# Kernel tuning notes

Measured on AMD Instinct MI355X. Metric: run time of the kernel, lower is better.

## Reference

```python
import jax, jax.numpy as jnp
import numpy as np

N, E, F, H = 50000, 1600000, 128, 128  # nodes, edges, input_nf, hidden_nf


def setup_inputs() -> dict:
    key = jax.random.key(0)
    ks = jax.random.split(key, 16)
    s = 0.05
    inp = {
        "h": jax.random.normal(ks[0], (N, F), jnp.float32),
        "coord": jax.random.normal(ks[1], (N, 3), jnp.float32),
        "edge_index": jax.random.randint(ks[2], (2, E), 0, N, jnp.int32),
        # edge_mlp: Linear(2F+1, H) -> SiLU -> Linear(H, H) -> SiLU
        "We1": jax.random.normal(ks[3], (2 * F + 1, H), jnp.float32) * s,
        "be1": jnp.zeros((H,), jnp.float32),
        "We2": jax.random.normal(ks[4], (H, H), jnp.float32) * s,
        "be2": jnp.zeros((H,), jnp.float32),
        # node_mlp: Linear(H+F, H) -> SiLU -> Linear(H, F)
        "Wn1": jax.random.normal(ks[5], (H + F, H), jnp.float32) * s,
        "bn1": jnp.zeros((H,), jnp.float32),
        "Wn2": jax.random.normal(ks[6], (H, F), jnp.float32) * s,
        "bn2": jnp.zeros((F,), jnp.float32),
        # coord_mlp: Linear(H, H) -> SiLU -> Linear(H, 1, bias=False) (xavier gain 0.001)
        "Wc1": jax.random.normal(ks[7], (H, H), jnp.float32) * s,
        "bc1": jnp.zeros((H,), jnp.float32),
        "Wc2": jax.random.normal(ks[8], (H, 1), jnp.float32) * 0.001,
    }
    return inp


def reference(h, coord, edge_index, We1, be1, We2, be2, Wn1, bn1, Wn2, bn2, Wc1, bc1, Wc2):
    row, col = edge_index[0], edge_index[1]
    n = h.shape[0]

    # coord2radial (normalize=False)
    coord_diff = coord[row] - coord[col]                      # [E, 3]
    radial = jnp.sum(coord_diff * coord_diff, axis=1, keepdims=True)  # [E, 1]

    # edge_model (attention=False, edge_attr=None)
    e_in = jnp.concatenate([h[row], h[col], radial], axis=1)  # [E, 2F+1]
    edge_feat = jax.nn.silu(jax.nn.silu(e_in @ We1 + be1) @ We2 + be2)  # [E, H]

    # coord_model (coords_agg='mean', reflection_equiv=True, tanh=False)
    phi = jax.nn.silu(edge_feat @ Wc1 + bc1) @ Wc2            # [E, 1]
    trans = coord_diff * phi                                   # [E, 3]
    agg_c = jax.ops.segment_sum(trans, row, num_segments=n)    # [N, 3]
    cnt = jax.ops.segment_sum(jnp.ones((trans.shape[0], 1), trans.dtype), row, num_segments=n)
    coord_out = coord + agg_c / jnp.maximum(cnt, 1.0)

    # node_model (node_attr=None, residual=True)
    agg_h = jax.ops.segment_sum(edge_feat, row, num_segments=n)  # [N, H]
    n_in = jnp.concatenate([h, agg_h], axis=1)                   # [N, F+H]
    h_out = h + (jax.nn.silu(n_in @ Wn1 + bn1) @ Wn2 + bn2)

    return h_out, coord_out
```

## Files before the change

### kernel.cpp

```cpp
#include <hip/hip_runtime.h>


typedef float f32x4 __attribute__((ext_vector_type(4)));
typedef short s16x8 __attribute__((ext_vector_type(8)));

#define NN   50000
#define EE   1600000
#define NHF  6400000
#define NBIN 50000
#define NT   25000

__device__ __forceinline__ unsigned short f2bf(float x){
  union { float f; unsigned int u; } v; v.f = x;
  unsigned int r = v.u + 0x7fffu + ((v.u >> 16) & 1u);
  return (unsigned short)(r >> 16);
}
__device__ __forceinline__ unsigned int pack2(float a, float b){
  unsigned int r;
  asm("v_cvt_pk_bf16_f32 %0, %1, %2" : "=v"(r) : "v"(a), "v"(b));
  return r;
}
__device__ __forceinline__ float silu_f(float x){
  return x * __builtin_amdgcn_rcpf(1.f + __expf(-x));
}
__device__ __forceinline__ float bflo(unsigned int u){ return __uint_as_float(u << 16); }
__device__ __forceinline__ float bfhi(unsigned int u){ return __uint_as_float(u & 0xffff0000u); }

__device__ __forceinline__ f32x4 mfma16(s16x8 a, s16x8 b, f32x4 c){
  return __builtin_amdgcn_mfma_f32_16x16x32_bf16(a, b, c, 0, 0, 0);
}

template<int CTRL> __device__ __forceinline__ float dppf(float x){
  return __int_as_float(__builtin_amdgcn_update_dpp(0, __float_as_int(x), CTRL, 0xF, 0xF, true));
}
template<int CTRL> __device__ __forceinline__ int dppi(int x){
  return __builtin_amdgcn_update_dpp(-1, x, CTRL, 0xF, 0xF, false);
}

__device__ __forceinline__ short* sptr(short* base, int fi, int slot){
  return (short*)((char*)base + (fi << 10) + (((slot << 4) ^ ((fi & 3) << 5))));
}

__global__ void pack_weights(const float* __restrict__ We1, const float* __restrict__ We2,
                             const float* __restrict__ Wc1, const float* __restrict__ Wn1,
                             const float* __restrict__ Wn2, short* __restrict__ wp)
{
  int b = blockIdx.x;
  int m = b >> 5, t = b & 31;
  int ft = t >> 2, ks = t & 3;
  int lane = threadIdx.x;
  const float* src;
  switch (m) {
    case 0: src = We1;            break;
    case 1: src = We1 + 128*128;  break;
    case 2: src = We2;            break;
    case 3: src = Wc1;            break;
    case 4: src = Wn1;            break;
    case 5: src = Wn1 + 128*128;  break;
    default: src = Wn2;           break;
  }
  short* dst = wp + m*16384 + (((ft<<2) + ks)*64 + lane)*8;
  int f  = (ft<<4) + (lane & 15);
  int kb = (ks<<5) + ((lane >> 4) << 3);
#pragma unroll
  for (int j = 0; j < 8; ++j)
    dst[j] = (short)f2bf(src[(kb + j)*128 + f]);
}

__global__ __launch_bounds__(256, 2)
void a1_kernel(const float* __restrict__ h32, const short* __restrict__ wp,
               unsigned short* __restrict__ A1)
{
  __shared__ short sA[16][64][8];
  const int tid = threadIdx.x, w = tid >> 6, lane = tid & 63;
  const int n0 = blockIdx.x << 6;
  const int el = tid >> 2, q = tid & 3;
  const int fi0 = ((el >> 4) << 2) + q, er = el & 15;
  {
    const int node = n0 + el;
    if (node < NN) {
      const float* hp = h32 + (size_t)node*128 + q*32;
#pragma unroll
      for (int lg = 0; lg < 4; ++lg) {
        f32x4 u = *(const f32x4*)(hp + lg*8);
        f32x4 v = *(const f32x4*)(hp + lg*8 + 4);
        uint4 o;
        o.x = pack2(u.x, u.y); o.y = pack2(u.z, u.w);
        o.z = pack2(v.x, v.y); o.w = pack2(v.z, v.w);
        *(uint4*)&sA[fi0][lg*16 + er][0] = o;
      }
    } else {
      s16x8 z = {};
#pragma unroll
      for (int lg = 0; lg < 4; ++lg) *(s16x8*)&sA[fi0][lg*16 + er][0] = z;
    }
  }
  __syncthreads();

  static const int wpm[3] = {0, 1, 4};
#pragma unroll
  for (int p = 0; p < 2; ++p) {
    s16x8 af[3][4];
#pragma unroll
    for (int j = 0; j < 3; ++j) {
      const int ftg = w*6 + p*3 + j;
      const int mi = ftg >> 3, fti = ftg & 7;
#pragma unroll
      for (int ks = 0; ks < 4; ++ks)
        af[j][ks] = *(const s16x8*)(wp + wpm[mi]*16384 + (((fti<<2) + ks)*64 + lane)*8);
    }
    f32x4 acc[3][4] = {};
#pragma unroll
    for (int et = 0; et < 4; ++et)
#pragma unroll
      for (int ks = 0; ks < 4; ++ks) {
        s16x8 b = *(const s16x8*)&sA[et*4+ks][lane][0];
#pragma unroll
        for (int j = 0; j < 3; ++j)
          acc[j][et] = mfma16(af[j][ks], b, acc[j][et]);
      }
#pragma unroll
    for (int j = 0; j < 3; ++j) {
      const int ftg = w*6 + p*3 + j;
#pragma unroll
      for (int et = 0; et < 4; ++et) {
        const int node = n0 + et*16 + (lane & 15);
        if (node < NN) {
          f32x4 a = acc[j][et];
          uint2 o; o.x = pack2(a.x, a.y); o.y = pack2(a.z, a.w);
          *(uint2*)(A1 + (size_t)node*384 + ftg*16 + ((lane >> 4) << 2)) = o;
        }
      }
    }
  }
}

__global__ void hist_k(const int* __restrict__ eidx, int* __restrict__ hist)
{
  int e = blockIdx.x*256 + threadIdx.x;
  if (e < EE) atomicAdd(&hist[eidx[e]], 1);
}

__global__ void scan_k(const int* __restrict__ hist, int* __restrict__ cur)
{
  __shared__ int s_a[256];
  const int t = threadIdx.x;
  const int lo = t * 196;
  const int hi = (lo + 196 < NBIN) ? lo + 196 : NBIN;
  int s = 0;
  for (int i = lo; i < hi; ++i) s += hist[i];
  s_a[t] = s;
  __syncthreads();
  int acc = s;
#pragma unroll
  for (int d = 1; d < 256; d <<= 1) {
    int u = (t >= d) ? s_a[t - d] : 0;
    __syncthreads();
    acc += u;
    s_a[t] = acc;
    __syncthreads();
  }
  int run = acc - s;
  for (int i = lo; i < hi; ++i) { cur[i] = run; run += hist[i]; }
}

__global__ void scatter_k(const int* __restrict__ eidx, int* __restrict__ cur,
                          int* __restrict__ perm)
{
  int e = blockIdx.x*256 + threadIdx.x;
  if (e < EE) {
    int p = atomicAdd(&cur[eidx[e]], 1);
    perm[p] = e;
  }
}

__global__ __launch_bounds__(256, 3)
void edge_kernel(const unsigned short* __restrict__ A1, const float* __restrict__ coord,
                 const int* __restrict__ eidx, const int* __restrict__ perm,
                 const short* __restrict__ wp,
                 const float* __restrict__ be1, const float* __restrict__ be2,
                 const float* __restrict__ bc1, const float* __restrict__ We1,
                 const float* __restrict__ Wc2,
                 float* __restrict__ aggh, float* __restrict__ aggc,
                 float* __restrict__ cntb)
{
  __shared__ short sAf[2][16*64*8];
  __shared__ float s_vec[5][128];
  __shared__ float s_rad[64];
  __shared__ float s_cd[64][3];
  __shared__ int   s_ri[64];
  __shared__ int   s_ci[64];
  __shared__ float s_phi[64];

  const int tid  = threadIdx.x;
  const int w    = tid >> 6, lane = tid & 63;
  const int ecol = lane & 15, rgrp = lane >> 4;

  if (tid < 128) {
    s_vec[0][tid] = be1[tid];
    s_vec[1][tid] = be2[tid];
    s_vec[2][tid] = bc1[tid];
    s_vec[3][tid] = We1[256*128 + tid];
    s_vec[4][tid] = Wc2[tid];
  }

  s16x8 wf2[2][4], wf3[2][4];
#pragma unroll
  for (int f2 = 0; f2 < 2; ++f2)
#pragma unroll
    for (int ks = 0; ks < 4; ++ks) {
      wf2[f2][ks] = *(const s16x8*)(wp + 2*16384 + ((((2*w+f2)<<2) + ks)*64 + lane)*8);
      wf3[f2][ks] = *(const s16x8*)(wp + 3*16384 + ((((2*w+f2)<<2) + ks)*64 + lane)*8);
    }

  short* sb0 = &sAf[0][0];
  short* sb1 = &sAf[1][0];

  const int tbeg = blockIdx.x * 13;
  const int tend = (tbeg + 13 < NT) ? tbeg + 13 : NT;

  for (int t = tbeg; t < tend; ++t) {
    const int e0 = t << 6;
    if (tid < 64) {
      int e = perm[e0 + tid];
      int r = eidx[e], c = eidx[EE + e];
      s_ri[tid] = r; s_ci[tid] = c;
      float ax = coord[3*r], ay = coord[3*r+1], az = coord[3*r+2];
      float bx = coord[3*c], by = coord[3*c+1], bz = coord[3*c+2];
      float dx = ax-bx, dy = ay-by, dz = az-bz;
      s_cd[tid][0] = dx; s_cd[tid][1] = dy; s_cd[tid][2] = dz;
      s_rad[tid] = dx*dx + dy*dy + dz*dz;
      s_phi[tid] = 0.f;
    }
    __syncthreads();

    {
      int rr[4], cc[4]; float rd[4];
#pragma unroll
      for (int et = 0; et < 4; ++et) {
        const int e_ = et*16 + ecol;
        rr[et] = s_ri[e_]; cc[et] = s_ci[e_]; rd[et] = s_rad[e_];
      }
      uint2 gr[2][4], gc[2][4];
#pragma unroll
      for (int f2 = 0; f2 < 2; ++f2) {
        const int f0 = (2*w+f2)*16 + (rgrp << 2);
#pragma unroll
        for (int et = 0; et < 4; ++et) {
          gr[f2][et] = *(const uint2*)(A1 + (size_t)rr[et]*384 + f0);
          gc[f2][et] = *(const uint2*)(A1 + (size_t)cc[et]*384 + 128 + f0);
        }
      }
#pragma unroll
      for (int f2 = 0; f2 < 2; ++f2) {
        const int f0 = (2*w+f2)*16 + (rgrp << 2);
        const int ks2 = f0 >> 5, lg2 = (f0 & 31) >> 3, j0 = f0 & 7;
        f32x4 w1c = *(const f32x4*)&s_vec[3][f0];
        f32x4 b1  = *(const f32x4*)&s_vec[0][f0];
#pragma unroll
        for (int et = 0; et < 4; ++et) {
          const uint2 r2v = gr[f2][et], c2v = gc[f2][et];
          f32x4 x;
          x.x = silu_f(bflo(r2v.x) + bflo(c2v.x) + rd[et]*w1c.x + b1.x);
          x.y = silu_f(bfhi(r2v.x) + bfhi(c2v.x) + rd[et]*w1c.y + b1.y);
          x.z = silu_f(bflo(r2v.y) + bflo(c2v.y) + rd[et]*w1c.z + b1.z);
          x.w = silu_f(bfhi(r2v.y) + bfhi(c2v.y) + rd[et]*w1c.w + b1.w);
          uint2 p; p.x = pack2(x.x, x.y); p.y = pack2(x.z, x.w);
          *(uint2*)((char*)sptr(sb0, et*4 + ks2, lg2*16 + ecol) + 2*j0) = p;
        }
      }
    }
    __syncthreads();

    f32x4 a2[2][4] = {};
#pragma unroll
    for (int et = 0; et < 4; ++et)
#pragma unroll
      for (int ks = 0; ks < 4; ++ks) {
        s16x8 b = *(const s16x8*)sptr(sb0, et*4+ks, lane);
        a2[0][et] = mfma16(wf2[0][ks], b, a2[0][et]);
        a2[1][et] = mfma16(wf2[1][ks], b, a2[1][et]);
      }
#pragma unroll
    for (int et = 0; et < 4; ++et) {
      const int r_l = s_ri[et*16 + ecol];
      f32x4 xx0, xx1;
#pragma unroll
      for (int f2 = 0; f2 < 2; ++f2) {
        const int f0 = (2*w+f2)*16 + (rgrp << 2);
        const int ks2 = f0 >> 5, lg2 = (f0 & 31) >> 3, j0 = f0 & 7;
        f32x4 b2 = *(const f32x4*)&s_vec[1][f0];
        f32x4 x = a2[f2][et];
        x.x = silu_f(x.x + b2.x); x.y = silu_f(x.y + b2.y);
        x.z = silu_f(x.z + b2.z); x.w = silu_f(x.w + b2.w);
        uint2 p; p.x = pack2(x.x, x.y); p.y = pack2(x.z, x.w);
        *(uint2*)((char*)sptr(sb1, et*4 + ks2, lg2*16 + ecol) + 2*j0) = p;
        if (f2 == 0) xx0 = x; else xx1 = x;
      }
#define SEG_ROUND(CTRL) { \
      int rn = dppi<CTRL>(r_l); \
      bool ok = (rn == r_l); \
      float u; \
      u = dppf<CTRL>(xx0.x); xx0.x += ok ? u : 0.f; \
      u = dppf<CTRL>(xx0.y); xx0.y += ok ? u : 0.f; \
      u = dppf<CTRL>(xx0.z); xx0.z += ok ? u : 0.f; \
      u = dppf<CTRL>(xx0.w); xx0.w += ok ? u : 0.f; \
      u = dppf<CTRL>(xx1.x); xx1.x += ok ? u : 0.f; \
      u = dppf<CTRL>(xx1.y); xx1.y += ok ? u : 0.f; \
      u = dppf<CTRL>(xx1.z); xx1.z += ok ? u : 0.f; \
      u = dppf<CTRL>(xx1.w); xx1.w += ok ? u : 0.f; }
      SEG_ROUND(0x101)
      SEG_ROUND(0x102)
      SEG_ROUND(0x104)
      SEG_ROUND(0x108)
#undef SEG_ROUND
      const int rprev = dppi<0x111>(r_l);
      if (rprev != r_l) {
        const int f0a = (2*w+0)*16 + (rgrp << 2);
        const int f0b = (2*w+1)*16 + (rgrp << 2);
        float* aga = aggh + (size_t)r_l*128 + f0a;
        float* agb = aggh + (size_t)r_l*128 + f0b;
        atomicAdd(aga+0, xx0.x); atomicAdd(aga+1, xx0.y);
        atomicAdd(aga+2, xx0.z); atomicAdd(aga+3, xx0.w);
        atomicAdd(agb+0, xx1.x); atomicAdd(agb+1, xx1.y);
        atomicAdd(agb+2, xx1.z); atomicAdd(agb+3, xx1.w);
      }
    }
    __syncthreads();

    f32x4 a3[2][4] = {};
#pragma unroll
    for (int et = 0; et < 4; ++et)
#pragma unroll
      for (int ks = 0; ks < 4; ++ks) {
        s16x8 b = *(const s16x8*)sptr(sb1, et*4+ks, lane);
        a3[0][et] = mfma16(wf3[0][ks], b, a3[0][et]);
        a3[1][et] = mfma16(wf3[1][ks], b, a3[1][et]);
      }
#pragma unroll
    for (int et = 0; et < 4; ++et) {
      float p = 0.f;
#pragma unroll
      for (int f2 = 0; f2 < 2; ++f2) {
        const int f0 = (2*w+f2)*16 + (rgrp << 2);
        f32x4 bc = *(const f32x4*)&s_vec[2][f0];
        f32x4 wc = *(const f32x4*)&s_vec[4][f0];
        f32x4 x = a3[f2][et];
        p += silu_f(x.x + bc.x)*wc.x + silu_f(x.y + bc.y)*wc.y
           + silu_f(x.z + bc.z)*wc.z + silu_f(x.w + bc.w)*wc.w;
      }
      p += __shfl_xor(p, 16);
      p += __shfl_xor(p, 32);
      if (rgrp == 0) atomicAdd(&s_phi[et*16 + ecol], p);
    }
    __syncthreads();

    if (tid < 64) {
      int r = s_ri[tid];
      float ph = s_phi[tid];
      float cx = s_cd[tid][0]*ph, cy = s_cd[tid][1]*ph, cz = s_cd[tid][2]*ph, c1 = 1.f;
#pragma unroll
      for (int d = 1; d < 64; d <<= 1) {
        const int sl = tid + d;
        int   r2 = __shfl(r,  sl, 64);
        float ux = __shfl(cx, sl, 64), uy = __shfl(cy, sl, 64);
        float uz = __shfl(cz, sl, 64), uw = __shfl(c1, sl, 64);
        if ((sl < 64) && (r2 == r)) { cx+=ux; cy+=uy; cz+=uz; c1+=uw; }
      }
      if (tid == 0 || s_ri[tid-1] != r) {
        atomicAdd(&aggc[3*r+0], cx); atomicAdd(&aggc[3*r+1], cy);
        atomicAdd(&aggc[3*r+2], cz); atomicAdd(&cntb[r], c1);
      }
    }
    __syncthreads();
  }
}

__global__ __launch_bounds__(256, 2)
void node_kernel(const unsigned short* __restrict__ A1, const float* __restrict__ h32,
                 const short* __restrict__ wp, const float* __restrict__ bn1,
                 const float* __restrict__ bn2, float* __restrict__ hout)
{
  __shared__ short sA[16][64][8];
  __shared__ float s_vec[2][128];
  const int tid  = threadIdx.x, w = tid >> 6, lane = tid & 63;
  const int ecol = lane & 15, rgrp = lane >> 4;
  if (tid < 128) { s_vec[0][tid] = bn1[tid]; s_vec[1][tid] = bn2[tid]; }

  s16x8 wfa[2][4], wfb[2][4];
#pragma unroll
  for (int f2 = 0; f2 < 2; ++f2)
#pragma unroll
    for (int ks = 0; ks < 4; ++ks) {
      wfa[f2][ks] = *(const s16x8*)(wp + 5*16384 + ((((2*w+f2)<<2) + ks)*64 + lane)*8);
      wfb[f2][ks] = *(const s16x8*)(wp + 6*16384 + ((((2*w+f2)<<2) + ks)*64 + lane)*8);
    }

  const int n0 = blockIdx.x << 6;
  const int el = tid >> 2, q = tid & 3;
  const int fi0 = ((el >> 4) << 2) + q, er = el & 15;
  {
    const int node = n0 + el;
    if (node < NN) {
      const float* ap = hout + (size_t)node*128 + q*32;
#pragma unroll
      for (int lg = 0; lg < 4; ++lg) {
        f32x4 u = *(const f32x4*)(ap + lg*8);
        f32x4 v = *(const f32x4*)(ap + lg*8 + 4);
        uint4 o;
        o.x = pack2(u.x, u.y); o.y = pack2(u.z, u.w);
        o.z = pack2(v.x, v.y); o.w = pack2(v.z, v.w);
        *(uint4*)&sA[fi0][lg*16 + er][0] = o;
      }
    } else {
      s16x8 z = {};
#pragma unroll
      for (int lg = 0; lg < 4; ++lg) *(s16x8*)&sA[fi0][lg*16 + er][0] = z;
    }
  }
  __syncthreads();

  f32x4 acc[2][4] = {};
#pragma unroll
  for (int et = 0; et < 4; ++et)
#pragma unroll
    for (int ks = 0; ks < 4; ++ks) {
      s16x8 ba = *(const s16x8*)&sA[et*4+ks][lane][0];
      acc[0][et] = mfma16(wfa[0][ks], ba, acc[0][et]);
      acc[1][et] = mfma16(wfa[1][ks], ba, acc[1][et]);
    }
  __syncthreads();

#pragma unroll
  for (int f2 = 0; f2 < 2; ++f2) {
    const int ft = 2*w + f2, f0 = ft*16 + (rgrp << 2);
    const int ks2 = f0 >> 5, lg2 = (f0 & 31) >> 3, j0 = f0 & 7;
    f32x4 b1 = *(const f32x4*)&s_vec[0][f0];
#pragma unroll
    for (int et = 0; et < 4; ++et) {
      const int node = n0 + et*16 + ecol;
      uint2 g = {0u, 0u};
      if (node < NN) g = *(const uint2*)(A1 + (size_t)node*384 + 256 + f0);
      f32x4 x = acc[f2][et];
      x.x = silu_f(x.x + bflo(g.x) + b1.x);
      x.y = silu_f(x.y + bfhi(g.x) + b1.y);
      x.z = silu_f(x.z + bflo(g.y) + b1.z);
      x.w = silu_f(x.w + bfhi(g.y) + b1.w);
      uint2 p; p.x = pack2(x.x, x.y); p.y = pack2(x.z, x.w);
      *(uint2*)&sA[et*4 + ks2][lg2*16 + ecol][j0] = p;
    }
  }
  __syncthreads();

  f32x4 a2[2][4] = {};
#pragma unroll
  for (int et = 0; et < 4; ++et)
#pragma unroll
    for (int ks = 0; ks < 4; ++ks) {
      s16x8 b = *(const s16x8*)&sA[et*4+ks][lane][0];
      a2[0][et] = mfma16(wfb[0][ks], b, a2[0][et]);
      a2[1][et] = mfma16(wfb[1][ks], b, a2[1][et]);
    }
#pragma unroll
  for (int f2 = 0; f2 < 2; ++f2) {
    const int f0 = (2*w+f2)*16 + (rgrp << 2);
    f32x4 b2 = *(const f32x4*)&s_vec[1][f0];
#pragma unroll
    for (int et = 0; et < 4; ++et) {
      const int node = n0 + et*16 + ecol;
      if (node < NN) {
        f32x4 hv = *(const f32x4*)(h32 + (size_t)node*128 + f0);
        f32x4 x = a2[f2][et];
        x.x += b2.x + hv.x; x.y += b2.y + hv.y;
        x.z += b2.z + hv.z; x.w += b2.w + hv.w;
        *(f32x4*)(hout + (size_t)node*128 + f0) = x;
      }
    }
  }
}

__global__ void coord_kernel(const float* __restrict__ coord, const float* __restrict__ aggc,
                             const float* __restrict__ cntb, float* __restrict__ out)
{
  int i = blockIdx.x*256 + threadIdx.x;
  if (i < NN) {
    float inv = __builtin_amdgcn_rcpf(fmaxf(cntb[i], 1.f));
    out[NHF + 3*i+0] = coord[3*i+0] + aggc[3*i+0]*inv;
    out[NHF + 3*i+1] = coord[3*i+1] + aggc[3*i+1]*inv;
    out[NHF + 3*i+2] = coord[3*i+2] + aggc[3*i+2]*inv;
  }
}

extern "C" void kernel_launch(void* const* d_in, const int* in_sizes, int n_in,
                              void* d_out, int out_size, void* d_ws, size_t ws_size,
                              hipStream_t stream)
{
  (void)in_sizes; (void)n_in; (void)out_size; (void)ws_size;
  const float* h    = (const float*)d_in[0];
  const float* crd  = (const float*)d_in[1];
  const int*   eidx = (const int*)  d_in[2];
  const float* We1  = (const float*)d_in[3];
  const float* be1  = (const float*)d_in[4];
  const float* We2  = (const float*)d_in[5];
  const float* be2  = (const float*)d_in[6];
  const float* Wn1  = (const float*)d_in[7];
  const float* bn1  = (const float*)d_in[8];
  const float* Wn2  = (const float*)d_in[9];
  const float* bn2  = (const float*)d_in[10];
  const float* Wc1  = (const float*)d_in[11];
  const float* bc1  = (const float*)d_in[12];
  const float* Wc2  = (const float*)d_in[13];
  float* out = (float*)d_out;
  char*  ws  = (char*)d_ws;

  short*          wp   = (short*)ws;
  unsigned short* A1   = (unsigned short*)(ws + 229376);
  float*          aggc = (float*)(ws + 38629376);
  float*          cntb = (float*)(ws + 39229376);
  int*            hist = (int*)  (ws + 39429376);
  int*            cur  = (int*)  (ws + 39629376);
  int*            perm = (int*)  (ws + 39829376);

  hipMemsetAsync(out, 0, (size_t)NHF*4, stream);
  hipMemsetAsync(ws + 38629376, 0, 800000, stream);
  hipMemsetAsync(ws + 39429376, 0, 200000, stream);

  pack_weights<<<dim3(224), dim3(64), 0, stream>>>(We1, We2, Wc1, Wn1, Wn2, wp);
  a1_kernel<<<dim3(782), dim3(256), 0, stream>>>(h, wp, A1);
  hist_k<<<dim3(6250), dim3(256), 0, stream>>>(eidx, hist);
  scan_k<<<dim3(1), dim3(256), 0, stream>>>(hist, cur);
  scatter_k<<<dim3(6250), dim3(256), 0, stream>>>(eidx, cur, perm);
  edge_kernel<<<dim3(1924), dim3(256), 0, stream>>>(A1, crd, eidx, perm, wp,
                                                    be1, be2, bc1, We1, Wc2,
                                                    out, aggc, cntb);
  node_kernel<<<dim3(782), dim3(256), 0, stream>>>(A1, h, wp, bn1, bn2, out);
  coord_kernel<<<dim3(196), dim3(256), 0, stream>>>(crd, aggc, cntb, out);
}
```

Before: 783.5 us.

## Software-pipeline edge gathers across tiles and parallelize the bucket prefix scan

The edge kernel now loads the next tile's row and column indices, coordinates and bf16 A1 gathers into registers and double-buffered shared arrays while the current tile runs its MFMA stages. One trailing barrier per iteration is removed because the per-tile shared state alternates between two buffers. The single-block serial scan is replaced by a three-kernel block-parallel scan, and the segmented DPP reduction uses a multiply-by-mask instead of selects. The changes trade extra registers, which may lower occupancy, and two extra launches for hidden gather latency and a shorter scan.

```diff
diff --git a/kernel.cpp b/kernel.cpp
--- a/kernel.cpp
+++ b/kernel.cpp
@@ -141,27 +141,45 @@
   if (e < EE) atomicAdd(&hist[eidx[e]], 1);
 }
 
-__global__ void scan_k(const int* __restrict__ hist, int* __restrict__ cur)
-{
-  __shared__ int s_a[256];
+__global__ void scanA(const int* __restrict__ hist, int* __restrict__ cur,
+                      int* __restrict__ btot)
+{
+  __shared__ int s[256];
   const int t = threadIdx.x;
-  const int lo = t * 196;
-  const int hi = (lo + 196 < NBIN) ? lo + 196 : NBIN;
-  int s = 0;
-  for (int i = lo; i < hi; ++i) s += hist[i];
-  s_a[t] = s;
-  __syncthreads();
-  int acc = s;
+  const int i = blockIdx.x*256 + t;
+  int v = (i < NBIN) ? hist[i] : 0;
+  s[t] = v; __syncthreads();
+  int acc = v;
 #pragma unroll
   for (int d = 1; d < 256; d <<= 1) {
-    int u = (t >= d) ? s_a[t - d] : 0;
-    __syncthreads();
-    acc += u;
-    s_a[t] = acc;
-    __syncthreads();
-  }
-  int run = acc - s;
-  for (int i = lo; i < hi; ++i) { cur[i] = run; run += hist[i]; }
+    int u = (t >= d) ? s[t - d] : 0;
+    __syncthreads();
+    acc += u; s[t] = acc;
+    __syncthreads();
+  }
+  if (i < NBIN) cur[i] = acc - v;
+  if (t == 255) btot[blockIdx.x] = acc;
+}
+__global__ void scanB(int* __restrict__ btot)
+{
+  __shared__ int s[256];
+  const int t = threadIdx.x;
+  int v = (t < 196) ? btot[t] : 0;
+  s[t] = v; __syncthreads();
+  int acc = v;
+#pragma unroll
+  for (int d = 1; d < 256; d <<= 1) {
+    int u = (t >= d) ? s[t - d] : 0;
+    __syncthreads();
+    acc += u; s[t] = acc;
+    __syncthreads();
+  }
+  if (t < 196) btot[t] = acc - v;
+}
+__global__ void scanC(int* __restrict__ cur, const int* __restrict__ btot)
+{
+  int i = blockIdx.x*256 + threadIdx.x;
+  if (i < NBIN) cur[i] += btot[blockIdx.x];
 }
 
 __global__ void scatter_k(const int* __restrict__ eidx, int* __restrict__ cur,
@@ -186,11 +204,10 @@
 {
   __shared__ short sAf[2][16*64*8];
   __shared__ float s_vec[5][128];
-  __shared__ float s_rad[64];
-  __shared__ float s_cd[64][3];
-  __shared__ int   s_ri[64];
-  __shared__ int   s_ci[64];
-  __shared__ float s_phi[64];
+  __shared__ float s_rad[2][64];
+  __shared__ float s_cd[2][64][3];
+  __shared__ int   s_ri[2][64];
+  __shared__ float s_phi[2][64];
 
   const int tid  = threadIdx.x;
   const int w    = tid >> 6, lane = tid & 63;
@@ -218,56 +235,75 @@
 
   const int tbeg = blockIdx.x * 13;
   const int tend = (tbeg + 13 < NT) ? tbeg + 13 : NT;
-
-  for (int t = tbeg; t < tend; ++t) {
-    const int e0 = t << 6;
+  if (tbeg >= NT) return;
+
+  uint2 grA[2][4], gcA[2][4];
+  {
+    const int e0 = tbeg << 6;
     if (tid < 64) {
       int e = perm[e0 + tid];
       int r = eidx[e], c = eidx[EE + e];
-      s_ri[tid] = r; s_ci[tid] = c;
+      s_ri[0][tid] = r;
       float ax = coord[3*r], ay = coord[3*r+1], az = coord[3*r+2];
       float bx = coord[3*c], by = coord[3*c+1], bz = coord[3*c+2];
       float dx = ax-bx, dy = ay-by, dz = az-bz;
-      s_cd[tid][0] = dx; s_cd[tid][1] = dy; s_cd[tid][2] = dz;
-      s_rad[tid] = dx*dx + dy*dy + dz*dz;
-      s_phi[tid] = 0.f;
-    }
-    __syncthreads();
-
-    {
-      int rr[4], cc[4]; float rd[4];
+      s_cd[0][tid][0] = dx; s_cd[0][tid][1] = dy; s_cd[0][tid][2] = dz;
+      s_rad[0][tid] = dx*dx + dy*dy + dz*dz;
+      s_phi[0][tid] = 0.f;
+    }
+    int rr[4], cc[4];
+#pragma unroll
+    for (int et = 0; et < 4; ++et) {
+      int e = perm[e0 + et*16 + ecol];
+      rr[et] = eidx[e]; cc[et] = eidx[EE + e];
+    }
+#pragma unroll
+    for (int f2 = 0; f2 < 2; ++f2) {
+      const int f0 = (2*w+f2)*16 + (rgrp << 2);
 #pragma unroll
       for (int et = 0; et < 4; ++et) {
-        const int e_ = et*16 + ecol;
-        rr[et] = s_ri[e_]; cc[et] = s_ci[e_]; rd[et] = s_rad[e_];
-      }
-      uint2 gr[2][4], gc[2][4];
-#pragma unroll
-      for (int f2 = 0; f2 < 2; ++f2) {
-        const int f0 = (2*w+f2)*16 + (rgrp << 2);
-#pragma unroll
-        for (int et = 0; et < 4; ++et) {
-          gr[f2][et] = *(const uint2*)(A1 + (size_t)rr[et]*384 + f0);
-          gc[f2][et] = *(const uint2*)(A1 + (size_t)cc[et]*384 + 128 + f0);
-        }
-      }
-#pragma unroll
-      for (int f2 = 0; f2 < 2; ++f2) {
-        const int f0 = (2*w+f2)*16 + (rgrp << 2);
-        const int ks2 = f0 >> 5, lg2 = (f0 & 31) >> 3, j0 = f0 & 7;
-        f32x4 w1c = *(const f32x4*)&s_vec[3][f0];
-        f32x4 b1  = *(const f32x4*)&s_vec[0][f0];
-#pragma unroll
-        for (int et = 0; et < 4; ++et) {
-          const uint2 r2v = gr[f2][et], c2v = gc[f2][et];
-          f32x4 x;
-          x.x = silu_f(bflo(r2v.x) + bflo(c2v.x) + rd[et]*w1c.x + b1.x);
-          x.y = silu_f(bfhi(r2v.x) + bfhi(c2v.x) + rd[et]*w1c.y + b1.y);
-          x.z = silu_f(bflo(r2v.y) + bflo(c2v.y) + rd[et]*w1c.z + b1.z);
-          x.w = silu_f(bfhi(r2v.y) + bfhi(c2v.y) + rd[et]*w1c.w + b1.w);
-          uint2 p; p.x = pack2(x.x, x.y); p.y = pack2(x.z, x.w);
-          *(uint2*)((char*)sptr(sb0, et*4 + ks2, lg2*16 + ecol) + 2*j0) = p;
-        }
+        grA[f2][et] = *(const uint2*)(A1 + (size_t)rr[et]*384 + f0);
+        gcA[f2][et] = *(const uint2*)(A1 + (size_t)cc[et]*384 + 128 + f0);
+      }
+    }
+  }
+  __syncthreads();
+
+  int pb = 0;
+  for (int t = tbeg; t < tend; ++t, pb ^= 1) {
+    const int nb = pb ^ 1;
+    const int tn = (t+1 < tend) ? t+1 : t;
+    const int e1 = tn << 6;
+
+    int prr[4], pcc[4];
+#pragma unroll
+    for (int et = 0; et < 4; ++et) {
+      int e = perm[e1 + et*16 + ecol];
+      prr[et] = eidx[e]; pcc[et] = eidx[EE + e];
+    }
+    int nr = 0, ncn = 0;
+    if (tid < 64) {
+      int e = perm[e1 + tid];
+      nr = eidx[e]; ncn = eidx[EE + e];
+    }
+
+#pragma unroll
+    for (int f2 = 0; f2 < 2; ++f2) {
+      const int f0 = (2*w+f2)*16 + (rgrp << 2);
+      const int ks2 = f0 >> 5, lg2 = (f0 & 31) >> 3, j0 = f0 & 7;
+      f32x4 w1c = *(const f32x4*)&s_vec[3][f0];
+      f32x4 b1  = *(const f32x4*)&s_vec[0][f0];
+#pragma unroll
+      for (int et = 0; et < 4; ++et) {
+        float rad = s_rad[pb][et*16 + ecol];
+        const uint2 rv = grA[f2][et], cv = gcA[f2][et];
+        f32x4 x;
+        x.x = silu_f(bflo(rv.x) + bflo(cv.x) + rad*w1c.x + b1.x);
+        x.y = silu_f(bfhi(rv.x) + bfhi(cv.x) + rad*w1c.y + b1.y);
+        x.z = silu_f(bflo(rv.y) + bflo(cv.y) + rad*w1c.z + b1.z);
+        x.w = silu_f(bfhi(rv.y) + bfhi(cv.y) + rad*w1c.w + b1.w);
+        uint2 p; p.x = pack2(x.x, x.y); p.y = pack2(x.z, x.w);
+        *(uint2*)((char*)sptr(sb0, et*4 + ks2, lg2*16 + ecol) + 2*j0) = p;
       }
     }
     __syncthreads();
@@ -281,9 +317,29 @@
         a2[0][et] = mfma16(wf2[0][ks], b, a2[0][et]);
         a2[1][et] = mfma16(wf2[1][ks], b, a2[1][et]);
       }
+
+#pragma unroll
+    for (int f2 = 0; f2 < 2; ++f2) {
+      const int f0 = (2*w+f2)*16 + (rgrp << 2);
+#pragma unroll
+      for (int et = 0; et < 4; ++et) {
+        grA[f2][et] = *(const uint2*)(A1 + (size_t)prr[et]*384 + f0);
+        gcA[f2][et] = *(const uint2*)(A1 + (size_t)pcc[et]*384 + 128 + f0);
+      }
+    }
+    if (tid < 64) {
+      s_ri[nb][tid] = nr;
+      float ax = coord[3*nr], ay = coord[3*nr+1], az = coord[3*nr+2];
+      float bx = coord[3*ncn], by = coord[3*ncn+1], bz = coord[3*ncn+2];
+      float dx = ax-bx, dy = ay-by, dz = az-bz;
+      s_cd[nb][tid][0] = dx; s_cd[nb][tid][1] = dy; s_cd[nb][tid][2] = dz;
+      s_rad[nb][tid] = dx*dx + dy*dy + dz*dz;
+      s_phi[nb][tid] = 0.f;
+    }
+
 #pragma unroll
     for (int et = 0; et < 4; ++et) {
-      const int r_l = s_ri[et*16 + ecol];
+      const int r_l = s_ri[pb][et*16 + ecol];
       f32x4 xx0, xx1;
 #pragma unroll
       for (int f2 = 0; f2 < 2; ++f2) {
@@ -299,16 +355,15 @@
       }
 #define SEG_ROUND(CTRL) { \
       int rn = dppi<CTRL>(r_l); \
-      bool ok = (rn == r_l); \
-      float u; \
-      u = dppf<CTRL>(xx0.x); xx0.x += ok ? u : 0.f; \
-      u = dppf<CTRL>(xx0.y); xx0.y += ok ? u : 0.f; \
-      u = dppf<CTRL>(xx0.z); xx0.z += ok ? u : 0.f; \
-      u = dppf<CTRL>(xx0.w); xx0.w += ok ? u : 0.f; \
-      u = dppf<CTRL>(xx1.x); xx1.x += ok ? u : 0.f; \
-      u = dppf<CTRL>(xx1.y); xx1.y += ok ? u : 0.f; \
-      u = dppf<CTRL>(xx1.z); xx1.z += ok ? u : 0.f; \
-      u = dppf<CTRL>(xx1.w); xx1.w += ok ? u : 0.f; }
+      float m = (rn == r_l) ? 1.f : 0.f; \
+      xx0.x += dppf<CTRL>(xx0.x)*m; \
+      xx0.y += dppf<CTRL>(xx0.y)*m; \
+      xx0.z += dppf<CTRL>(xx0.z)*m; \
+      xx0.w += dppf<CTRL>(xx0.w)*m; \
+      xx1.x += dppf<CTRL>(xx1.x)*m; \
+      xx1.y += dppf<CTRL>(xx1.y)*m; \
+      xx1.z += dppf<CTRL>(xx1.z)*m; \
+      xx1.w += dppf<CTRL>(xx1.w)*m; }
       SEG_ROUND(0x101)
       SEG_ROUND(0x102)
       SEG_ROUND(0x104)
@@ -351,14 +406,15 @@
       }
       p += __shfl_xor(p, 16);
       p += __shfl_xor(p, 32);
-      if (rgrp == 0) atomicAdd(&s_phi[et*16 + ecol], p);
+      if (rgrp == 0) atomicAdd(&s_phi[pb][et*16 + ecol], p);
     }
     __syncthreads();
 
     if (tid < 64) {
-      int r = s_ri[tid];
-      float ph = s_phi[tid];
-      float cx = s_cd[tid][0]*ph, cy = s_cd[tid][1]*ph, cz = s_cd[tid][2]*ph, c1 = 1.f;
+      int r = s_ri[pb][tid];
+      float ph = s_phi[pb][tid];
+      float cx = s_cd[pb][tid][0]*ph, cy = s_cd[pb][tid][1]*ph;
+      float cz = s_cd[pb][tid][2]*ph, c1 = 1.f;
 #pragma unroll
       for (int d = 1; d < 64; d <<= 1) {
         const int sl = tid + d;
@@ -367,12 +423,11 @@
         float uz = __shfl(cz, sl, 64), uw = __shfl(c1, sl, 64);
         if ((sl < 64) && (r2 == r)) { cx+=ux; cy+=uy; cz+=uz; c1+=uw; }
       }
-      if (tid == 0 || s_ri[tid-1] != r) {
+      if (tid == 0 || s_ri[pb][tid-1] != r) {
         atomicAdd(&aggc[3*r+0], cx); atomicAdd(&aggc[3*r+1], cy);
         atomicAdd(&aggc[3*r+2], cz); atomicAdd(&cntb[r], c1);
       }
     }
-    __syncthreads();
   }
 }
 
@@ -519,7 +574,8 @@
   float*          cntb = (float*)(ws + 39229376);
   int*            hist = (int*)  (ws + 39429376);
   int*            cur  = (int*)  (ws + 39629376);
-  int*            perm = (int*)  (ws + 39829376);
+  int*            btot = (int*)  (ws + 39829376);
+  int*            perm = (int*)  (ws + 39830400);
 
   hipMemsetAsync(out, 0, (size_t)NHF*4, stream);
   hipMemsetAsync(ws + 38629376, 0, 800000, stream);
@@ -528,7 +584,9 @@
   pack_weights<<<dim3(224), dim3(64), 0, stream>>>(We1, We2, Wc1, Wn1, Wn2, wp);
   a1_kernel<<<dim3(782), dim3(256), 0, stream>>>(h, wp, A1);
   hist_k<<<dim3(6250), dim3(256), 0, stream>>>(eidx, hist);
-  scan_k<<<dim3(1), dim3(256), 0, stream>>>(hist, cur);
+  scanA<<<dim3(196), dim3(256), 0, stream>>>(hist, cur, btot);
+  scanB<<<dim3(1), dim3(256), 0, stream>>>(btot);
+  scanC<<<dim3(196), dim3(256), 0, stream>>>(cur, btot);
   scatter_k<<<dim3(6250), dim3(256), 0, stream>>>(eidx, cur, perm);
   edge_kernel<<<dim3(1924), dim3(256), 0, stream>>>(A1, crd, eidx, perm, wp,
                                                     be1, be2, bc1, We1, Wc2,
```

New measurement: 873.6 us. +11.5%, slower.
